# Performance work log

Hardware: AMD Instinct MI355X
Metric: run time of the kernel (lower is better)

## Reference

```python
import jax, jax.numpy as jnp
import numpy as np

E, B, F_IN = 24, 8192, 15
H1, H2, H3 = 512, 512, 256


def setup_inputs() -> dict:
    key = jax.random.key(0)
    ks = jax.random.split(key, 6)
    return {
        "features": jax.random.normal(ks[0], (B, F_IN), dtype=jnp.float32),
        "model_index": jax.random.randint(ks[1], (B,), 0, E, dtype=jnp.int32),
        "W1": jax.random.normal(ks[2], (E, F_IN, H1), dtype=jnp.float32) * 0.1,
        "b1": jnp.zeros((E, H1), dtype=jnp.float32),
        "W2": jax.random.normal(ks[3], (E, H1, H2), dtype=jnp.float32) * 0.05,
        "b2": jnp.zeros((E, H2), dtype=jnp.float32),
        "W3": jax.random.normal(ks[4], (E, H2, H3), dtype=jnp.float32) * 0.05,
        "b3": jnp.zeros((E, H3), dtype=jnp.float32),
        "W4": jax.random.normal(ks[5], (E, H3, 1), dtype=jnp.float32) * 0.05,
        "b4": jnp.zeros((E, 1), dtype=jnp.float32),
    }


def reference(features, model_index, W1, b1, W2, b2, W3, b3, W4, b4):
    # Run every expert MLP over the full batch (as the original does), then
    # gather the selected expert's output per sample.
    h = jax.nn.relu(jnp.einsum("bi,eih->ebh", features, W1) + b1[:, None, :])  # [E,B,H1]
    h = jax.nn.relu(jnp.einsum("ebh,ehk->ebk", h, W2) + b2[:, None, :])        # [E,B,H2]
    h = jax.nn.relu(jnp.einsum("ebk,ekm->ebm", h, W3) + b3[:, None, :])        # [E,B,H3]
    stacked = jnp.einsum("ebm,emo->ebo", h, W4) + b4[:, None, :]               # [E,B,1]
    # gather_nd equivalent: pick expert model_index[b] for each sample b
    out = stacked[model_index, jnp.arange(stacked.shape[1])]                   # [B,1]
    return out
```

## Files before the change

### kernel.cpp

```cpp
#include <hip/hip_runtime.h>

#define NE 24
#define NB 8192
#define FIN 15
#define H1 512
#define H2 512
#define H3 256
#define TS 32
#define SLOTS 260
#define GRIDM (8 * SLOTS)
#define PACKBLK 4803

#define WS_OFF 0
#define WS_XN  32
#define WS_XT  64
#define WS_ORD 4096
#define WB_BYTE 65536
#define OW1 0
#define OW2 393216
#define OW3 6684672
#define OW4 9830400

typedef __attribute__((ext_vector_type(8))) short short8v;
typedef __attribute__((ext_vector_type(4))) float f32x4;

__device__ __forceinline__ unsigned short f2bf(float x) {
  unsigned int u = __float_as_uint(x);
  unsigned int r = (u + 0x7fffu + ((u >> 16) & 1u)) >> 16;
  return (unsigned short)r;
}
__device__ __forceinline__ float bf2f(unsigned short h) {
  return __uint_as_float(((unsigned int)h) << 16);
}

__global__ __launch_bounds__(256) void k_pack(
    const float* __restrict__ W1, const float* __restrict__ W2,
    const float* __restrict__ W3, const float* __restrict__ W4,
    const int* __restrict__ midx, int* __restrict__ ws,
    unsigned short* __restrict__ wb) {
  const int t = threadIdx.x;
  if (blockIdx.x == PACKBLK) {
    __shared__ int hist[NE];
    __shared__ int off[NE + 1];
    __shared__ int cur[NE];
    __shared__ int tb[NE];
    __shared__ int xn[8];
    if (t < NE) hist[t] = 0;
    __syncthreads();
    int ev[32];
    #pragma unroll
    for (int r = 0; r < 32; ++r) {
      ev[r] = midx[r * 256 + t];
      atomicAdd(&hist[ev[r]], 1);
    }
    __syncthreads();
    if (t == 0) {
      int o = 0;
      #pragma unroll
      for (int i = 0; i < NE; ++i) { off[i] = o; cur[i] = o; o += hist[i]; }
      off[NE] = o;
    }
    if (t >= 32 && t < 40) {
      const int x = t - 32;
      int o = 0;
      for (int i = x; i < NE; i += 8) { tb[i] = o; o += (hist[i] + TS - 1) / TS; }
      xn[x] = o;
    }
    __syncthreads();
    if (t < NE + 1) ws[WS_OFF + t] = off[t];
    if (t >= 32 && t < 40) ws[WS_XN + t - 32] = xn[t - 32];
    for (int e = 0; e < NE; ++e) {
      const int nt = (hist[e] + TS - 1) / TS;
      for (int k = t; k < nt; k += 256)
        ws[WS_XT + (e & 7) * SLOTS + tb[e] + k] = (e << 16) | k;
    }
    #pragma unroll
    for (int r = 0; r < 32; ++r) {
      const int p = atomicAdd(&cur[ev[r]], 1);
      ws[WS_ORD + p] = r * 256 + t;
    }
    return;
  }
  int g = blockIdx.x * 256 + t;
  const float* src;
  unsigned short* dst;
  int Kb, N, KR;
  if (g < 49152) {
    src = W1; dst = wb + OW1; Kb = 4; N = 512; KR = 15;
  } else if (g < 49152 + 786432) {
    g -= 49152; src = W2; dst = wb + OW2; Kb = 64; N = 512; KR = 512;
  } else if (g < 49152 + 786432 + 393216) {
    g -= 49152 + 786432; src = W3; dst = wb + OW3; Kb = 64; N = 256; KR = 512;
  } else {
    g -= 49152 + 786432 + 393216; src = W4; dst = wb + OW4; Kb = 32; N = 1; KR = 256;
  }
  int e = g / (Kb * N);
  int r = g % (Kb * N);
  int kb = r / N;
  int n = r % N;
  short8v v;
  #pragma unroll
  for (int j = 0; j < 8; ++j) {
    int k = kb * 8 + j;
    float f = (k < KR) ? src[((size_t)e * KR + k) * N + n] : 0.f;
    v[j] = (short)f2bf(f);
  }
  *(short8v*)(dst + (size_t)g * 8) = v;
}

template <int NT, int KS>
__device__ __forceinline__ void layer_gemm(const unsigned short* __restrict__ aLDS,
                                           const unsigned short* __restrict__ bGlob,
                                           const float* __restrict__ bias,
                                           unsigned short* __restrict__ dLDS,
                                           int N, int ncol0, int lr, int lc) {
  f32x4 acc[2][NT];
  #pragma unroll
  for (int mt = 0; mt < 2; ++mt)
    #pragma unroll
    for (int nt = 0; nt < NT; ++nt) acc[mt][nt] = (f32x4){0.f, 0.f, 0.f, 0.f};

  const unsigned short* bbase = bGlob + ((size_t)lc * N + ncol0 + lr) * 8;
  const size_t kstep = (size_t)4 * N * 8;

  short8v bb[4][NT];
  #pragma unroll
  for (int p = 0; p < 3; ++p) {
    if (p < KS) {
      #pragma unroll
      for (int nt = 0; nt < NT; ++nt)
        bb[p][nt] = *(const short8v*)(bbase + p * kstep + nt * 128);
    }
  }
  #pragma unroll
  for (int ks = 0; ks < KS; ++ks) {
    if (ks + 3 < KS) {
      #pragma unroll
      for (int nt = 0; nt < NT; ++nt)
        bb[(ks + 3) & 3][nt] = *(const short8v*)(bbase + (ks + 3) * kstep + nt * 128);
    }
    const unsigned short* ap = aLDS + (((ks * 4 + lc) * 32) + lr) * 8;
    short8v a0 = *(const short8v*)ap;
    short8v a1 = *(const short8v*)(ap + 128);
    #pragma unroll
    for (int nt = 0; nt < NT; ++nt) {
      acc[0][nt] = __builtin_amdgcn_mfma_f32_16x16x32_bf16(a0, bb[ks & 3][nt], acc[0][nt], 0, 0, 0);
      acc[1][nt] = __builtin_amdgcn_mfma_f32_16x16x32_bf16(a1, bb[ks & 3][nt], acc[1][nt], 0, 0, 0);
    }
  }
  #pragma unroll
  for (int nt = 0; nt < NT; ++nt) {
    const int col = ncol0 + nt * 16 + lr;
    const float bb2 = bias[col];
    #pragma unroll
    for (int mt = 0; mt < 2; ++mt) {
      #pragma unroll
      for (int j = 0; j < 4; ++j) {
        const int row = mt * 16 + lc * 4 + j;
        const float v = fmaxf(acc[mt][nt][j] + bb2, 0.f);
        dLDS[(((col >> 3) * 32) + row) * 8 + (col & 7)] = f2bf(v);
      }
    }
  }
}

__global__ __launch_bounds__(512) void k_mlp(
    const float* __restrict__ features,
    const float* __restrict__ b1, const float* __restrict__ b2,
    const float* __restrict__ b3, const float* __restrict__ b4,
    const int* __restrict__ ws, const unsigned short* __restrict__ wb,
    float* __restrict__ out) {
  __shared__ int sidx[TS];
  __shared__ __align__(16) unsigned short fA[4][TS][8];
  __shared__ __align__(16) unsigned short actA[64][TS][8];
  __shared__ __align__(16) unsigned short actB[64][TS][8];

  const int t = threadIdx.x;
  const int wv = t >> 6;
  const int ln = t & 63;
  const int lr = ln & 15;
  const int lc = ln >> 4;

  const int bid = blockIdx.x;
  const int xcd = bid & 7;
  const int slot = bid >> 3;
  if (slot >= ws[WS_XN + xcd]) return;
  const int packed = ws[WS_XT + xcd * SLOTS + slot];
  const int e = packed >> 16;
  const int tt = packed & 0xffff;
  const int start = ws[WS_OFF + e] + tt * TS;
  const int cnt = min(TS, ws[WS_OFF + e + 1] - start);

  if (t < TS) sidx[t] = (t < cnt) ? ws[WS_ORD + start + t] : ws[WS_ORD + start];
  __syncthreads();

  if (t < 128) {
    int m = t >> 2, cb = t & 3;
    #pragma unroll
    for (int j = 0; j < 8; ++j) {
      int k = cb * 8 + j;
      fA[cb][m][j] = (k < FIN) ? f2bf(features[(size_t)sidx[m] * FIN + k]) : 0;
    }
  }
  __syncthreads();

  const unsigned short* w1p = wb + OW1 + (size_t)e * 4 * 512 * 8;
  const unsigned short* w2p = wb + OW2 + (size_t)e * 64 * 512 * 8;
  const unsigned short* w3p = wb + OW3 + (size_t)e * 64 * 256 * 8;
  const unsigned short* w4p = wb + OW4 + (size_t)e * 256;

  layer_gemm<4, 1>(&fA[0][0][0], w1p, b1 + e * H1, &actA[0][0][0], 512, wv * 64, lr, lc);
  __syncthreads();
  layer_gemm<4, 16>(&actA[0][0][0], w2p, b2 + e * H2, &actB[0][0][0], 512, wv * 64, lr, lc);
  __syncthreads();
  layer_gemm<2, 16>(&actB[0][0][0], w3p, b3 + e * H3, &actA[0][0][0], 256, wv * 32, lr, lc);
  __syncthreads();

  if (t < 256) {
    int m = t >> 3, c = t & 7;
    float p = 0.f;
    #pragma unroll
    for (int kk = 0; kk < 32; ++kk)
      p += bf2f(actA[0][0][(kk * 32 + m) * 8 + c]) * bf2f(w4p[kk * 8 + c]);
    p += __shfl_xor(p, 1);
    p += __shfl_xor(p, 2);
    p += __shfl_xor(p, 4);
    if (c == 0 && m < cnt) out[sidx[m]] = p + b4[e];
  }
}

extern "C" void kernel_launch(void* const* d_in, const int* in_sizes, int n_in,
                              void* d_out, int out_size, void* d_ws, size_t ws_size,
                              hipStream_t stream) {
  const float* features = (const float*)d_in[0];
  const int* midx = (const int*)d_in[1];
  const float* W1 = (const float*)d_in[2];
  const float* b1 = (const float*)d_in[3];
  const float* W2 = (const float*)d_in[4];
  const float* b2 = (const float*)d_in[5];
  const float* W3 = (const float*)d_in[6];
  const float* b3 = (const float*)d_in[7];
  const float* W4 = (const float*)d_in[8];
  const float* b4 = (const float*)d_in[9];
  int* ws = (int*)d_ws;
  unsigned short* wb = (unsigned short*)((char*)d_ws + WB_BYTE);
  float* out = (float*)d_out;

  k_pack<<<PACKBLK + 1, 256, 0, stream>>>(W1, W2, W3, W4, midx, ws, wb);
  k_mlp<<<GRIDM, 512, 0, stream>>>(features, b1, b2, b3, b4, ws, wb, out);
}
```

Measured before the change: 128.6 us.

## Double per-block sample tile to 64 rows for more weight reuse

```diff
diff --git a/kernel.cpp b/kernel.cpp
--- a/kernel.cpp
+++ b/kernel.cpp
@@ -6,8 +6,8 @@
 #define H1 512
 #define H2 512
 #define H3 256
-#define TS 32
-#define SLOTS 260
+#define TS 64
+#define SLOTS 130
 #define GRIDM (8 * SLOTS)
 #define PACKBLK 4803
 
@@ -108,15 +108,15 @@
   *(short8v*)(dst + (size_t)g * 8) = v;
 }
 
-template <int NT, int KS>
+template <int NT, int KS, int MT>
 __device__ __forceinline__ void layer_gemm(const unsigned short* __restrict__ aLDS,
                                            const unsigned short* __restrict__ bGlob,
                                            const float* __restrict__ bias,
                                            unsigned short* __restrict__ dLDS,
                                            int N, int ncol0, int lr, int lc) {
-  f32x4 acc[2][NT];
-  #pragma unroll
-  for (int mt = 0; mt < 2; ++mt)
+  f32x4 acc[MT][NT];
+  #pragma unroll
+  for (int mt = 0; mt < MT; ++mt)
     #pragma unroll
     for (int nt = 0; nt < NT; ++nt) acc[mt][nt] = (f32x4){0.f, 0.f, 0.f, 0.f};
 
@@ -139,32 +139,33 @@
       for (int nt = 0; nt < NT; ++nt)
         bb[(ks + 3) & 3][nt] = *(const short8v*)(bbase + (ks + 3) * kstep + nt * 128);
     }
-    const unsigned short* ap = aLDS + (((ks * 4 + lc) * 32) + lr) * 8;
-    short8v a0 = *(const short8v*)ap;
-    short8v a1 = *(const short8v*)(ap + 128);
-    #pragma unroll
-    for (int nt = 0; nt < NT; ++nt) {
-      acc[0][nt] = __builtin_amdgcn_mfma_f32_16x16x32_bf16(a0, bb[ks & 3][nt], acc[0][nt], 0, 0, 0);
-      acc[1][nt] = __builtin_amdgcn_mfma_f32_16x16x32_bf16(a1, bb[ks & 3][nt], acc[1][nt], 0, 0, 0);
-    }
+    const unsigned short* ap = aLDS + (((ks * 4 + lc) * TS) + lr) * 8;
+    short8v a[MT];
+    #pragma unroll
+    for (int mt = 0; mt < MT; ++mt) a[mt] = *(const short8v*)(ap + mt * 128);
+    #pragma unroll
+    for (int nt = 0; nt < NT; ++nt)
+      #pragma unroll
+      for (int mt = 0; mt < MT; ++mt)
+        acc[mt][nt] = __builtin_amdgcn_mfma_f32_16x16x32_bf16(a[mt], bb[ks & 3][nt], acc[mt][nt], 0, 0, 0);
   }
   #pragma unroll
   for (int nt = 0; nt < NT; ++nt) {
     const int col = ncol0 + nt * 16 + lr;
-    const float bb2 = bias[col];
-    #pragma unroll
-    for (int mt = 0; mt < 2; ++mt) {
+    const float bv = bias[col];
+    #pragma unroll
+    for (int mt = 0; mt < MT; ++mt) {
       #pragma unroll
       for (int j = 0; j < 4; ++j) {
         const int row = mt * 16 + lc * 4 + j;
-        const float v = fmaxf(acc[mt][nt][j] + bb2, 0.f);
-        dLDS[(((col >> 3) * 32) + row) * 8 + (col & 7)] = f2bf(v);
+        const float v = fmaxf(acc[mt][nt][j] + bv, 0.f);
+        dLDS[(((col >> 3) * TS) + row) * 8 + (col & 7)] = f2bf(v);
       }
     }
   }
 }
 
-__global__ __launch_bounds__(512) void k_mlp(
+__global__ __launch_bounds__(512, 2) void k_mlp(
     const float* __restrict__ features,
     const float* __restrict__ b1, const float* __restrict__ b2,
     const float* __restrict__ b3, const float* __restrict__ b4,
@@ -194,7 +195,7 @@
   if (t < TS) sidx[t] = (t < cnt) ? ws[WS_ORD + start + t] : ws[WS_ORD + start];
   __syncthreads();
 
-  if (t < 128) {
+  if (t < 256) {
     int m = t >> 2, cb = t & 3;
     #pragma unroll
     for (int j = 0; j < 8; ++j) {
@@ -209,19 +210,19 @@
   const unsigned short* w3p = wb + OW3 + (size_t)e * 64 * 256 * 8;
   const unsigned short* w4p = wb + OW4 + (size_t)e * 256;
 
-  layer_gemm<4, 1>(&fA[0][0][0], w1p, b1 + e * H1, &actA[0][0][0], 512, wv * 64, lr, lc);
-  __syncthreads();
-  layer_gemm<4, 16>(&actA[0][0][0], w2p, b2 + e * H2, &actB[0][0][0], 512, wv * 64, lr, lc);
-  __syncthreads();
-  layer_gemm<2, 16>(&actB[0][0][0], w3p, b3 + e * H3, &actA[0][0][0], 256, wv * 32, lr, lc);
-  __syncthreads();
-
-  if (t < 256) {
+  layer_gemm<4, 1, 4>(&fA[0][0][0], w1p, b1 + e * H1, &actA[0][0][0], 512, wv * 64, lr, lc);
+  __syncthreads();
+  layer_gemm<4, 16, 4>(&actA[0][0][0], w2p, b2 + e * H2, &actB[0][0][0], 512, wv * 64, lr, lc);
+  __syncthreads();
+  layer_gemm<2, 16, 4>(&actB[0][0][0], w3p, b3 + e * H3, &actA[0][0][0], 256, wv * 32, lr, lc);
+  __syncthreads();
+
+  {
     int m = t >> 3, c = t & 7;
     float p = 0.f;
     #pragma unroll
     for (int kk = 0; kk < 32; ++kk)
-      p += bf2f(actA[0][0][(kk * 32 + m) * 8 + c]) * bf2f(w4p[kk * 8 + c]);
+      p += bf2f(actA[0][0][(kk * TS + m) * 8 + c]) * bf2f(w4p[kk * 8 + c]);
     p += __shfl_xor(p, 1);
     p += __shfl_xor(p, 2);
     p += __shfl_xor(p, 4);
```

New measurement: 130.5 us. No clear change (+1.5%).

## Halve row tile to 16, single-MFMA-tile GEMM, XCD-aligned weight packing

Applied to the files above, without the earlier changes.

```diff
diff --git a/kernel.cpp b/kernel.cpp
--- a/kernel.cpp
+++ b/kernel.cpp
@@ -6,15 +6,16 @@
 #define H1 512
 #define H2 512
 #define H3 256
-#define TS 32
-#define SLOTS 260
+#define TS 16
+#define SLOTS 520
 #define GRIDM (8 * SLOTS)
-#define PACKBLK 4803
+#define EPB 201
+#define PACKBLK (8 * 3 * EPB)
 
 #define WS_OFF 0
 #define WS_XN  32
 #define WS_XT  64
-#define WS_ORD 4096
+#define WS_ORD 8192
 #define WB_BYTE 65536
 #define OW1 0
 #define OW2 393216
@@ -81,31 +82,42 @@
     }
     return;
   }
-  int g = blockIdx.x * 256 + t;
+  const int x = blockIdx.x & 7;
+  const int s = blockIdx.x >> 3;
+  const int e = x + 8 * (s / EPB);
+  const int gl = (s % EPB) * 256 + t;
+  if (gl >= 51232) return;
   const float* src;
-  unsigned short* dst;
-  int Kb, N, KR;
-  if (g < 49152) {
-    src = W1; dst = wb + OW1; Kb = 4; N = 512; KR = 15;
-  } else if (g < 49152 + 786432) {
-    g -= 49152; src = W2; dst = wb + OW2; Kb = 64; N = 512; KR = 512;
-  } else if (g < 49152 + 786432 + 393216) {
-    g -= 49152 + 786432; src = W3; dst = wb + OW3; Kb = 64; N = 256; KR = 512;
+  int kb, n, N, KR;
+  size_t dsto;
+  if (gl < 2048) {
+    kb = gl >> 9; n = gl & 511; N = 512; KR = FIN;
+    src = W1 + (size_t)e * FIN * 512;
+    dsto = OW1 + ((size_t)e * 2048 + gl) * 8;
+  } else if (gl < 34816) {
+    const int g2 = gl - 2048;
+    kb = g2 >> 9; n = g2 & 511; N = 512; KR = 512;
+    src = W2 + (size_t)e * 512 * 512;
+    dsto = OW2 + ((size_t)e * 32768 + g2) * 8;
+  } else if (gl < 51200) {
+    const int g3 = gl - 34816;
+    kb = g3 >> 8; n = g3 & 255; N = 256; KR = 512;
+    src = W3 + (size_t)e * 512 * 256;
+    dsto = OW3 + ((size_t)e * 16384 + g3) * 8;
   } else {
-    g -= 49152 + 786432 + 393216; src = W4; dst = wb + OW4; Kb = 32; N = 1; KR = 256;
-  }
-  int e = g / (Kb * N);
-  int r = g % (Kb * N);
-  int kb = r / N;
-  int n = r % N;
+    const int g4 = gl - 51200;
+    kb = g4; n = 0; N = 1; KR = 256;
+    src = W4 + (size_t)e * 256;
+    dsto = OW4 + (size_t)e * 256 + (size_t)g4 * 8;
+  }
   short8v v;
   #pragma unroll
   for (int j = 0; j < 8; ++j) {
-    int k = kb * 8 + j;
-    float f = (k < KR) ? src[((size_t)e * KR + k) * N + n] : 0.f;
+    const int k = kb * 8 + j;
+    const float f = (k < KR) ? src[(size_t)k * N + n] : 0.f;
     v[j] = (short)f2bf(f);
   }
-  *(short8v*)(dst + (size_t)g * 8) = v;
+  *(short8v*)(wb + dsto) = v;
 }
 
 template <int NT, int KS>
@@ -114,11 +126,9 @@
                                            const float* __restrict__ bias,
                                            unsigned short* __restrict__ dLDS,
                                            int N, int ncol0, int lr, int lc) {
-  f32x4 acc[2][NT];
-  #pragma unroll
-  for (int mt = 0; mt < 2; ++mt)
-    #pragma unroll
-    for (int nt = 0; nt < NT; ++nt) acc[mt][nt] = (f32x4){0.f, 0.f, 0.f, 0.f};
+  f32x4 acc[NT];
+  #pragma unroll
+  for (int nt = 0; nt < NT; ++nt) acc[nt] = (f32x4){0.f, 0.f, 0.f, 0.f};
 
   const unsigned short* bbase = bGlob + ((size_t)lc * N + ncol0 + lr) * 8;
   const size_t kstep = (size_t)4 * N * 8;
@@ -139,32 +149,25 @@
       for (int nt = 0; nt < NT; ++nt)
         bb[(ks + 3) & 3][nt] = *(const short8v*)(bbase + (ks + 3) * kstep + nt * 128);
     }
-    const unsigned short* ap = aLDS + (((ks * 4 + lc) * 32) + lr) * 8;
-    short8v a0 = *(const short8v*)ap;
-    short8v a1 = *(const short8v*)(ap + 128);
-    #pragma unroll
-    for (int nt = 0; nt < NT; ++nt) {
-      acc[0][nt] = __builtin_amdgcn_mfma_f32_16x16x32_bf16(a0, bb[ks & 3][nt], acc[0][nt], 0, 0, 0);
-      acc[1][nt] = __builtin_amdgcn_mfma_f32_16x16x32_bf16(a1, bb[ks & 3][nt], acc[1][nt], 0, 0, 0);
-    }
+    const short8v a = *(const short8v*)(aLDS + (((ks * 4 + lc) * TS) + lr) * 8);
+    #pragma unroll
+    for (int nt = 0; nt < NT; ++nt)
+      acc[nt] = __builtin_amdgcn_mfma_f32_16x16x32_bf16(a, bb[ks & 3][nt], acc[nt], 0, 0, 0);
   }
   #pragma unroll
   for (int nt = 0; nt < NT; ++nt) {
     const int col = ncol0 + nt * 16 + lr;
-    const float bb2 = bias[col];
-    #pragma unroll
-    for (int mt = 0; mt < 2; ++mt) {
-      #pragma unroll
-      for (int j = 0; j < 4; ++j) {
-        const int row = mt * 16 + lc * 4 + j;
-        const float v = fmaxf(acc[mt][nt][j] + bb2, 0.f);
-        dLDS[(((col >> 3) * 32) + row) * 8 + (col & 7)] = f2bf(v);
-      }
-    }
-  }
-}
-
-__global__ __launch_bounds__(512) void k_mlp(
+    const float bv = bias[col];
+    #pragma unroll
+    for (int j = 0; j < 4; ++j) {
+      const int row = lc * 4 + j;
+      const float v = fmaxf(acc[nt][j] + bv, 0.f);
+      dLDS[(((col >> 3) * TS) + row) * 8 + (col & 7)] = f2bf(v);
+    }
+  }
+}
+
+__global__ __launch_bounds__(512, 4) void k_mlp(
     const float* __restrict__ features,
     const float* __restrict__ b1, const float* __restrict__ b2,
     const float* __restrict__ b3, const float* __restrict__ b4,
@@ -194,7 +197,7 @@
   if (t < TS) sidx[t] = (t < cnt) ? ws[WS_ORD + start + t] : ws[WS_ORD + start];
   __syncthreads();
 
-  if (t < 128) {
+  if (t < 64) {
     int m = t >> 2, cb = t & 3;
     #pragma unroll
     for (int j = 0; j < 8; ++j) {
@@ -216,12 +219,12 @@
   layer_gemm<2, 16>(&actB[0][0][0], w3p, b3 + e * H3, &actA[0][0][0], 256, wv * 32, lr, lc);
   __syncthreads();
 
-  if (t < 256) {
+  if (t < 128) {
     int m = t >> 3, c = t & 7;
     float p = 0.f;
     #pragma unroll
     for (int kk = 0; kk < 32; ++kk)
-      p += bf2f(actA[0][0][(kk * 32 + m) * 8 + c]) * bf2f(w4p[kk * 8 + c]);
+      p += bf2f(actA[0][0][(kk * TS + m) * 8 + c]) * bf2f(w4p[kk * 8 + c]);
     p += __shfl_xor(p, 1);
     p += __shfl_xor(p, 2);
     p += __shfl_xor(p, 4);
```

Result: slower. 141.0 us (+9.7%).
